# Kernel tuning notes

Hardware: AMD Instinct MI355X
Metric: run time of the kernel (lower is better)

Reference implementation:

```python
import jax, jax.numpy as jnp
import numpy as np

N = 10000      # nodes
E = 320000     # edges (before self-loops)
D = 256        # d_model
DC = 128       # d_content = d_model // 2
L = 3          # num_layers
K = 4096       # nodes_of_interest
LN_EPS = 1e-5


def setup_inputs() -> dict:
    key = jax.random.key(0)
    ks = jax.random.split(key, 7)
    x = jax.random.normal(ks[0], (N, D), dtype=jnp.float32)
    edge_index = jax.random.randint(ks[1], (2, E), 0, N)
    nodes_of_interest = jax.random.randint(ks[2], (K,), 0, N)
    # per-layer linear weights (stacked over layers)
    Wc = jax.random.normal(ks[3], (L, DC, DC), dtype=jnp.float32) * (1.0 / np.sqrt(DC))
    bc = jnp.zeros((L, DC), dtype=jnp.float32)
    Wp = jax.random.normal(ks[4], (L, DC, DC), dtype=jnp.float32) * (1.0 / np.sqrt(DC))
    bp = jnp.zeros((L, DC), dtype=jnp.float32)
    gamma = jnp.ones((L, D), dtype=jnp.float32)
    beta = jnp.zeros((L, D), dtype=jnp.float32)
    return {"x": x, "edge_index": edge_index, "nodes_of_interest": nodes_of_interest,
            "Wc": Wc, "bc": bc, "Wp": Wp, "bp": bp, "gamma": gamma, "beta": beta}


def _layernorm(h, g, b):
    mu = jnp.mean(h, axis=-1, keepdims=True)
    var = jnp.mean((h - mu) ** 2, axis=-1, keepdims=True)
    return (h - mu) * jax.lax.rsqrt(var + LN_EPS) * g + b


def reference(x, edge_index, nodes_of_interest, Wc, bc, Wp, bp, gamma, beta):
    n = x.shape[0]
    loops = jnp.arange(n)
    # add self-loops (PyG add_self_loops): done per conv in torch but identical each layer
    row = jnp.concatenate([edge_index[0], loops])  # source j
    col = jnp.concatenate([edge_index[1], loops])  # target i
    # symmetric-ish normalization: degree counted over row only (as in source)
    deg = jax.ops.segment_sum(jnp.ones_like(row, dtype=x.dtype), row, num_segments=n)
    dis = deg ** -0.5
    norm = dis[row] * dis[col]  # [E+N]

    def conv(h, l):
        hc = h[:, :DC] @ Wc[l].T + bc[l]
        hp = h[:, DC:] @ Wp[l].T + bp[l]
        ht = jnp.concatenate([hc, hp], axis=-1)
        msg = norm[:, None] * ht[row]                      # gather + normalize
        return jax.ops.segment_sum(msg, col, num_segments=n)  # scatter-add

    for l in range(L - 1):
        x = x + jax.nn.relu(_layernorm(conv(x, l), gamma[l], beta[l]))
    x = x + _layernorm(conv(x, L - 1), gamma[L - 1], beta[L - 1])
    return x[nodes_of_interest]
```

## Files before the change

### kernel.cpp

```cpp
#include <hip/hip_runtime.h>

#define DMODEL 256
#define DCH 128
#define NLAYER 3
#define LN_EPS 1e-5f

typedef float f32x4 __attribute__((ext_vector_type(4)));
typedef short s16x8 __attribute__((ext_vector_type(8)));

__device__ __forceinline__ unsigned short f2bf(float f) {
  unsigned int u = __float_as_uint(f);
  unsigned int r = (u + 0x7FFF + ((u >> 16) & 1)) >> 16;
  return (unsigned short)r;
}
__device__ __forceinline__ unsigned int pk2bf(float x, float y) {
  return ((unsigned int)f2bf(y) << 16) | f2bf(x);
}
__device__ __forceinline__ float bflo(unsigned int u) { return __uint_as_float(u << 16); }
__device__ __forceinline__ float bfhi(unsigned int u) { return __uint_as_float(u & 0xFFFF0000u); }

__global__ __launch_bounds__(256) void hist_cvt_kernel(
    const int* __restrict__ row, const int* __restrict__ col,
    int* cnt_row, int* cnt_col, int E,
    const float* __restrict__ x, unsigned short* __restrict__ xbf, int nx8,
    const float* __restrict__ Wc, unsigned short* __restrict__ Wcb,
    const float* __restrict__ Wp, unsigned short* __restrict__ Wpb, int nw8) {
  int tid = blockIdx.x * 256 + threadIdx.x;
  if (tid < E) {
    atomicAdd(&cnt_row[row[tid]], 1);
    atomicAdd(&cnt_col[col[tid]], 1);
  }
  if (tid < nx8) {
    float4 a = *(const float4*)&x[tid * 8];
    float4 b = *(const float4*)&x[tid * 8 + 4];
    uint4 o = {pk2bf(a.x, a.y), pk2bf(a.z, a.w), pk2bf(b.x, b.y), pk2bf(b.z, b.w)};
    *(uint4*)&xbf[tid * 8] = o;
  }
  if (tid < nw8) {
    float4 a = *(const float4*)&Wc[tid * 8];
    float4 b = *(const float4*)&Wc[tid * 8 + 4];
    uint4 o = {pk2bf(a.x, a.y), pk2bf(a.z, a.w), pk2bf(b.x, b.y), pk2bf(b.z, b.w)};
    *(uint4*)&Wcb[tid * 8] = o;
    a = *(const float4*)&Wp[tid * 8];
    b = *(const float4*)&Wp[tid * 8 + 4];
    uint4 o2 = {pk2bf(a.x, a.y), pk2bf(a.z, a.w), pk2bf(b.x, b.y), pk2bf(b.z, b.w)};
    *(uint4*)&Wpb[tid * 8] = o2;
  }
}

__global__ __launch_bounds__(256) void scan_dis_kernel(
    const int* __restrict__ cnt_col, const int* __restrict__ cnt_row,
    int* __restrict__ indptr, int* __restrict__ cursor,
    float* __restrict__ dis, int N, int E) {
  int t = threadIdx.x;
  for (int i = t; i < N; i += 256) dis[i] = rsqrtf((float)(cnt_row[i] + 1));
  const int PER = (N + 255) / 256;
  int start = t * PER;
  int sum = 0;
  for (int k = 0; k < PER; ++k) {
    int i = start + k;
    if (i < N) sum += cnt_col[i];
  }
  int lane = t & 63, wid = t >> 6;
  int inc = sum;
#pragma unroll
  for (int off = 1; off < 64; off <<= 1) {
    int v = __shfl_up(inc, off);
    if (lane >= off) inc += v;
  }
  __shared__ int wsum[4];
  if (lane == 63) wsum[wid] = inc;
  __syncthreads();
  int woff = 0;
  for (int w = 0; w < wid; ++w) woff += wsum[w];
  int run = woff + inc - sum;
  for (int k = 0; k < PER; ++k) {
    int i = start + k;
    if (i < N) {
      indptr[i] = run;
      cursor[i] = run;
      run += cnt_col[i];
    }
  }
  if (t == 255) indptr[N] = E;
}

__global__ __launch_bounds__(256) void fill_kernel(const int* __restrict__ row,
    const int* __restrict__ col, int* cursor, int* __restrict__ idx, int E) {
  int e = blockIdx.x * 256 + threadIdx.x;
  if (e < E) {
    int pos = atomicAdd(&cursor[col[e]], 1);
    idx[pos] = row[e];
  }
}

__global__ __launch_bounds__(256) void agg_kernel(
    const unsigned short* __restrict__ xbf, unsigned short* __restrict__ S,
    float* __restrict__ swt, const float* __restrict__ dis,
    const int* __restrict__ indptr, const int* __restrict__ idx,
    const int* __restrict__ noi, int use_noi, int R) {
  int wave = threadIdx.x >> 6, lane = threadIdx.x & 63;
  int r = blockIdx.x * 4 + wave;
  int rc = min(r, R - 1);
  int i = use_noi ? noi[rc] : rc;
  float di = dis[i];
  float di2 = di * di;

  uint2 u = *(const uint2*)(xbf + (size_t)i * DMODEL + lane * 4);
  float a0 = di2 * bflo(u.x), a1 = di2 * bfhi(u.x);
  float a2 = di2 * bflo(u.y), a3 = di2 * bfhi(u.y);

  int s = indptr[i], e = indptr[i + 1];
  float sw = 0.f;
  for (int base = s; base < e; base += 64) {
    int n = min(64, e - base);
    int sr = 0;
    float w = 0.f;
    if (lane < n) {
      sr = idx[base + lane];
      w = dis[sr] * di;
    }
    int j = 0;
    for (; j + 4 <= n; j += 4) {
      int s0 = __shfl(sr, j), s1 = __shfl(sr, j + 1), s2 = __shfl(sr, j + 2), s3 = __shfl(sr, j + 3);
      float w0 = __shfl(w, j), w1 = __shfl(w, j + 1), w2 = __shfl(w, j + 2), w3 = __shfl(w, j + 3);
      uint2 u0 = *(const uint2*)(xbf + (size_t)s0 * DMODEL + lane * 4);
      uint2 u1 = *(const uint2*)(xbf + (size_t)s1 * DMODEL + lane * 4);
      uint2 u2 = *(const uint2*)(xbf + (size_t)s2 * DMODEL + lane * 4);
      uint2 u3 = *(const uint2*)(xbf + (size_t)s3 * DMODEL + lane * 4);
      a0 += w0 * bflo(u0.x); a1 += w0 * bfhi(u0.x); a2 += w0 * bflo(u0.y); a3 += w0 * bfhi(u0.y);
      a0 += w1 * bflo(u1.x); a1 += w1 * bfhi(u1.x); a2 += w1 * bflo(u1.y); a3 += w1 * bfhi(u1.y);
      a0 += w2 * bflo(u2.x); a1 += w2 * bfhi(u2.x); a2 += w2 * bflo(u2.y); a3 += w2 * bfhi(u2.y);
      a0 += w3 * bflo(u3.x); a1 += w3 * bfhi(u3.x); a2 += w3 * bflo(u3.y); a3 += w3 * bfhi(u3.y);
      sw += w0 + w1 + w2 + w3;
    }
    for (; j < n; ++j) {
      int sj = __shfl(sr, j);
      float wj = __shfl(w, j);
      uint2 uu = *(const uint2*)(xbf + (size_t)sj * DMODEL + lane * 4);
      a0 += wj * bflo(uu.x); a1 += wj * bfhi(uu.x); a2 += wj * bflo(uu.y); a3 += wj * bfhi(uu.y);
      sw += wj;
    }
  }
  if (r < R) {
    uint2 o = {pk2bf(a0, a1), pk2bf(a2, a3)};
    *(uint2*)(S + (size_t)r * DMODEL + lane * 4) = o;
    if (lane == 0) swt[r] = di2 + sw;
  }
}

__global__ __launch_bounds__(512) void xform_kernel(
    const unsigned short* __restrict__ S, const float* __restrict__ swt,
    const unsigned short* __restrict__ Wcb, const unsigned short* __restrict__ Wpb,
    const float* __restrict__ bc, const float* __restrict__ bp,
    const float* __restrict__ gamma, const float* __restrict__ beta,
    const float* __restrict__ xin, const int* __restrict__ noi,
    float* __restrict__ xout, unsigned short* __restrict__ xbf_out,
    int use_noi, int relu, int R) {
  int t = threadIdx.x;
  int w = t >> 6, lane = t & 63;
  int mt = w & 1, cq = w >> 1;
  int h = cq >> 1, cgg = cq & 1;
  int lrow = lane & 15, kgrp = lane >> 4;
  int r0 = blockIdx.x * 32;

  int arow = r0 + mt * 16 + lrow;
  int arow_c = min(arow, R - 1);
  const unsigned short* ap = S + (size_t)arow_c * DMODEL + h * DCH + kgrp * 8;
  const unsigned short* Wh = h ? Wpb : Wcb;
  const float* bh = h ? bp : bc;

  int orow0 = mt * 16 + kgrp * 4;
  float sj[4];
#pragma unroll
  for (int j = 0; j < 4; ++j) sj[j] = swt[min(r0 + orow0 + j, R - 1)];

  int colw[4];
  const unsigned short* bpw[4];
  f32x4 acc[4];
#pragma unroll
  for (int nt = 0; nt < 4; ++nt) {
    colw[nt] = cgg * 64 + nt * 16 + lrow;
    bpw[nt] = Wh + (size_t)colw[nt] * DCH + kgrp * 8;
    float bias = bh[colw[nt]];
    acc[nt] = (f32x4){bias * sj[0], bias * sj[1], bias * sj[2], bias * sj[3]};
  }

  union U8 { s16x8 v; uint4 q; };
#pragma unroll
  for (int kt = 0; kt < 4; ++kt) {
    U8 af;
    af.q = *(const uint4*)(ap + kt * 32);
#pragma unroll
    for (int nt = 0; nt < 4; ++nt) {
      U8 bf;
      bf.q = *(const uint4*)(bpw[nt] + kt * 32);
      acc[nt] = __builtin_amdgcn_mfma_f32_16x16x32_bf16(af.v, bf.v, acc[nt], 0, 0, 0);
    }
  }

  float p1[4], p2[4];
#pragma unroll
  for (int j = 0; j < 4; ++j) {
    p1[j] = acc[0][j] + acc[1][j] + acc[2][j] + acc[3][j];
    p2[j] = acc[0][j] * acc[0][j] + acc[1][j] * acc[1][j] +
            acc[2][j] * acc[2][j] + acc[3][j] * acc[3][j];
  }
#pragma unroll
  for (int off = 8; off > 0; off >>= 1) {
#pragma unroll
    for (int j = 0; j < 4; ++j) {
      p1[j] += __shfl_down(p1[j], off, 16);
      p2[j] += __shfl_down(p2[j], off, 16);
    }
  }
  __shared__ float red1[32][4], red2[32][4];
  __shared__ float muS[32], rsS[32];
  if (lrow == 0) {
#pragma unroll
    for (int j = 0; j < 4; ++j) {
      red1[orow0 + j][cq] = p1[j];
      red2[orow0 + j][cq] = p2[j];
    }
  }
  __syncthreads();
  if (t < 32) {
    float s1 = red1[t][0] + red1[t][1] + red1[t][2] + red1[t][3];
    float s2 = red2[t][0] + red2[t][1] + red2[t][2] + red2[t][3];
    float mu = s1 * (1.0f / DMODEL);
    float var = s2 * (1.0f / DMODEL) - mu * mu;
    muS[t] = mu;
    rsS[t] = rsqrtf(var + LN_EPS);
  }
  __syncthreads();

#pragma unroll
  for (int nt = 0; nt < 4; ++nt) {
    int col = h * DCH + colw[nt];
    float g = gamma[col], bt = beta[col];
#pragma unroll
    for (int j = 0; j < 4; ++j) {
      int rr = orow0 + j;
      int grow = r0 + rr;
      if (grow < R) {
        float y = (acc[nt][j] - muS[rr]) * rsS[rr] * g + bt;
        if (relu) y = fmaxf(y, 0.f);
        int node = use_noi ? noi[grow] : grow;
        float o = xin[(size_t)node * DMODEL + col] + y;
        xout[(size_t)grow * DMODEL + col] = o;
        if (xbf_out) xbf_out[(size_t)grow * DMODEL + col] = f2bf(o);
      }
    }
  }
}

extern "C" void kernel_launch(void* const* d_in, const int* in_sizes, int n_in,
                              void* d_out, int out_size, void* d_ws, size_t ws_size,
                              hipStream_t stream) {
  const float* x     = (const float*)d_in[0];
  const int*   edges = (const int*)d_in[1];
  const int*   noi   = (const int*)d_in[2];
  const float* Wc    = (const float*)d_in[3];
  const float* bc    = (const float*)d_in[4];
  const float* Wp    = (const float*)d_in[5];
  const float* bp    = (const float*)d_in[6];
  const float* gamma = (const float*)d_in[7];
  const float* beta  = (const float*)d_in[8];

  int N = in_sizes[0] / DMODEL;
  int E = in_sizes[1] / 2;
  int K = in_sizes[2];
  int nwElem = in_sizes[3];
  const int* row = edges;
  const int* col = edges + E;

  char* base = (char*)d_ws;
  size_t off = 0;
  auto alloc = [&](size_t bytes) -> void* {
    void* p = base + off;
    off += (bytes + 255) & ~(size_t)255;
    return p;
  };

  unsigned short* xbf0   = (unsigned short*)alloc((size_t)N * DMODEL * 2);
  unsigned short* xbfA   = (unsigned short*)alloc((size_t)N * DMODEL * 2);
  unsigned short* xbfB   = (unsigned short*)alloc((size_t)N * DMODEL * 2);
  unsigned short* Sb     = (unsigned short*)alloc((size_t)N * DMODEL * 2);
  float*          xA     = (float*)alloc((size_t)N * DMODEL * 4);
  float*          xB     = (float*)alloc((size_t)N * DMODEL * 4);
  unsigned short* Wcb    = (unsigned short*)alloc((size_t)nwElem * 2);
  unsigned short* Wpb    = (unsigned short*)alloc((size_t)nwElem * 2);
  float*          swt    = (float*)alloc((size_t)N * 4);
  float*          dis    = (float*)alloc((size_t)N * 4);
  int*            cnt    = (int*)alloc((size_t)2 * N * 4);
  int*            indptr = (int*)alloc((size_t)(N + 1) * 4);
  int*            cursor = (int*)alloc((size_t)N * 4);
  int*            idx    = (int*)alloc((size_t)E * 4);

  hipMemsetAsync(cnt, 0, (size_t)2 * N * 4, stream);

  int nx8 = (N * DMODEL) / 8;
  int nw8 = nwElem / 8;
  int mx = E > nx8 ? E : nx8;
  if (nw8 > mx) mx = nw8;
  hist_cvt_kernel<<<(mx + 255) / 256, 256, 0, stream>>>(
      row, col, cnt, cnt + N, E, x, xbf0, nx8, Wc, Wcb, Wp, Wpb, nw8);
  scan_dis_kernel<<<1, 256, 0, stream>>>(cnt + N, cnt, indptr, cursor, dis, N, E);
  fill_kernel<<<(E + 255) / 256, 256, 0, stream>>>(row, col, cursor, idx, E);

  agg_kernel<<<(N + 3) / 4, 256, 0, stream>>>(xbf0, Sb, swt, dis, indptr, idx, nullptr, 0, N);
  xform_kernel<<<(N + 31) / 32, 512, 0, stream>>>(
      Sb, swt, Wcb, Wpb, bc, bp, gamma, beta, x, nullptr, xA, xbfA, 0, 1, N);
  agg_kernel<<<(N + 3) / 4, 256, 0, stream>>>(xbfA, Sb, swt, dis, indptr, idx, nullptr, 0, N);
  xform_kernel<<<(N + 31) / 32, 512, 0, stream>>>(
      Sb, swt, Wcb + (size_t)DCH * DCH, Wpb + (size_t)DCH * DCH, bc + DCH, bp + DCH,
      gamma + DMODEL, beta + DMODEL, xA, nullptr, xB, xbfB, 0, 1, N);
  agg_kernel<<<(K + 3) / 4, 256, 0, stream>>>(xbfB, Sb, swt, dis, indptr, idx, noi, 1, K);
  xform_kernel<<<(K + 31) / 32, 512, 0, stream>>>(
      Sb, swt, Wcb + (size_t)2 * DCH * DCH, Wpb + (size_t)2 * DCH * DCH, bc + 2 * DCH, bp + 2 * DCH,
      gamma + 2 * DMODEL, beta + 2 * DMODEL, xB, noi, (float*)d_out, nullptr, 1, 0, K);
}
```

Measured before the change: 265.5 us.

## Fuse neighbor aggregation and linear/LayerNorm transform into one per-layer kernel

Merges the gather-aggregate kernel and the MFMA transform+LayerNorm kernel into a single layer kernel. Each 512-thread block aggregates its 32 rows into LDS, where each wave handles 4 rows, and then runs the bf16 MFMA transform directly from that padded LDS tile. This removes the global round-trip of the aggregated S buffer and the swt buffer, plus three kernel launches. In exchange, each block has fewer independent gather waves in flight per row and higher LDS use, which could lower occupancy or latency hiding for the gather phase.

```diff
diff --git a/kernel.cpp b/kernel.cpp
--- a/kernel.cpp
+++ b/kernel.cpp
@@ -2,8 +2,8 @@
 
 #define DMODEL 256
 #define DCH 128
-#define NLAYER 3
 #define LN_EPS 1e-5f
+#define SROW (DMODEL + 8)
 
 typedef float f32x4 __attribute__((ext_vector_type(4)));
 typedef short s16x8 __attribute__((ext_vector_type(8)));
@@ -94,86 +94,85 @@
   }
 }
 
-__global__ __launch_bounds__(256) void agg_kernel(
-    const unsigned short* __restrict__ xbf, unsigned short* __restrict__ S,
-    float* __restrict__ swt, const float* __restrict__ dis,
-    const int* __restrict__ indptr, const int* __restrict__ idx,
-    const int* __restrict__ noi, int use_noi, int R) {
-  int wave = threadIdx.x >> 6, lane = threadIdx.x & 63;
-  int r = blockIdx.x * 4 + wave;
-  int rc = min(r, R - 1);
-  int i = use_noi ? noi[rc] : rc;
-  float di = dis[i];
-  float di2 = di * di;
-
-  uint2 u = *(const uint2*)(xbf + (size_t)i * DMODEL + lane * 4);
-  float a0 = di2 * bflo(u.x), a1 = di2 * bfhi(u.x);
-  float a2 = di2 * bflo(u.y), a3 = di2 * bfhi(u.y);
-
-  int s = indptr[i], e = indptr[i + 1];
-  float sw = 0.f;
-  for (int base = s; base < e; base += 64) {
-    int n = min(64, e - base);
-    int sr = 0;
-    float w = 0.f;
-    if (lane < n) {
-      sr = idx[base + lane];
-      w = dis[sr] * di;
-    }
-    int j = 0;
-    for (; j + 4 <= n; j += 4) {
-      int s0 = __shfl(sr, j), s1 = __shfl(sr, j + 1), s2 = __shfl(sr, j + 2), s3 = __shfl(sr, j + 3);
-      float w0 = __shfl(w, j), w1 = __shfl(w, j + 1), w2 = __shfl(w, j + 2), w3 = __shfl(w, j + 3);
-      uint2 u0 = *(const uint2*)(xbf + (size_t)s0 * DMODEL + lane * 4);
-      uint2 u1 = *(const uint2*)(xbf + (size_t)s1 * DMODEL + lane * 4);
-      uint2 u2 = *(const uint2*)(xbf + (size_t)s2 * DMODEL + lane * 4);
-      uint2 u3 = *(const uint2*)(xbf + (size_t)s3 * DMODEL + lane * 4);
-      a0 += w0 * bflo(u0.x); a1 += w0 * bfhi(u0.x); a2 += w0 * bflo(u0.y); a3 += w0 * bfhi(u0.y);
-      a0 += w1 * bflo(u1.x); a1 += w1 * bfhi(u1.x); a2 += w1 * bflo(u1.y); a3 += w1 * bfhi(u1.y);
-      a0 += w2 * bflo(u2.x); a1 += w2 * bfhi(u2.x); a2 += w2 * bflo(u2.y); a3 += w2 * bfhi(u2.y);
-      a0 += w3 * bflo(u3.x); a1 += w3 * bfhi(u3.x); a2 += w3 * bflo(u3.y); a3 += w3 * bfhi(u3.y);
-      sw += w0 + w1 + w2 + w3;
-    }
-    for (; j < n; ++j) {
-      int sj = __shfl(sr, j);
-      float wj = __shfl(w, j);
-      uint2 uu = *(const uint2*)(xbf + (size_t)sj * DMODEL + lane * 4);
-      a0 += wj * bflo(uu.x); a1 += wj * bfhi(uu.x); a2 += wj * bflo(uu.y); a3 += wj * bfhi(uu.y);
-      sw += wj;
-    }
-  }
-  if (r < R) {
-    uint2 o = {pk2bf(a0, a1), pk2bf(a2, a3)};
-    *(uint2*)(S + (size_t)r * DMODEL + lane * 4) = o;
-    if (lane == 0) swt[r] = di2 + sw;
-  }
-}
-
-__global__ __launch_bounds__(512) void xform_kernel(
-    const unsigned short* __restrict__ S, const float* __restrict__ swt,
+__global__ __launch_bounds__(512) void layer_kernel(
+    const unsigned short* __restrict__ xbf, const float* __restrict__ xres,
     const unsigned short* __restrict__ Wcb, const unsigned short* __restrict__ Wpb,
     const float* __restrict__ bc, const float* __restrict__ bp,
     const float* __restrict__ gamma, const float* __restrict__ beta,
-    const float* __restrict__ xin, const int* __restrict__ noi,
+    const float* __restrict__ dis, const int* __restrict__ indptr,
+    const int* __restrict__ idx, const int* __restrict__ noi,
     float* __restrict__ xout, unsigned short* __restrict__ xbf_out,
     int use_noi, int relu, int R) {
+  __shared__ unsigned short S_lds[32][SROW];
+  __shared__ float swt_lds[32];
+  __shared__ float red1[32][4], red2[32][4], muS[32], rsS[32];
+
   int t = threadIdx.x;
   int w = t >> 6, lane = t & 63;
+  int r0 = blockIdx.x * 32;
+
+  for (int q = 0; q < 4; ++q) {
+    int lr = w * 4 + q;
+    int r = r0 + lr;
+    if (r < R) {
+      int i = use_noi ? noi[r] : r;
+      float di = dis[i];
+      float di2 = di * di;
+      uint2 u = *(const uint2*)(xbf + (size_t)i * DMODEL + lane * 4);
+      float a0 = di2 * bflo(u.x), a1 = di2 * bfhi(u.x);
+      float a2 = di2 * bflo(u.y), a3 = di2 * bfhi(u.y);
+      int s = indptr[i], e = indptr[i + 1];
+      float sw = 0.f;
+      for (int base = s; base < e; base += 64) {
+        int n = min(64, e - base);
+        int sr = 0;
+        float wt = 0.f;
+        if (lane < n) {
+          sr = idx[base + lane];
+          wt = dis[sr] * di;
+        }
+        int j = 0;
+        for (; j + 4 <= n; j += 4) {
+          int s0 = __shfl(sr, j), s1 = __shfl(sr, j + 1), s2 = __shfl(sr, j + 2), s3 = __shfl(sr, j + 3);
+          float w0 = __shfl(wt, j), w1 = __shfl(wt, j + 1), w2 = __shfl(wt, j + 2), w3 = __shfl(wt, j + 3);
+          uint2 u0 = *(const uint2*)(xbf + (size_t)s0 * DMODEL + lane * 4);
+          uint2 u1 = *(const uint2*)(xbf + (size_t)s1 * DMODEL + lane * 4);
+          uint2 u2 = *(const uint2*)(xbf + (size_t)s2 * DMODEL + lane * 4);
+          uint2 u3 = *(const uint2*)(xbf + (size_t)s3 * DMODEL + lane * 4);
+          a0 += w0 * bflo(u0.x); a1 += w0 * bfhi(u0.x); a2 += w0 * bflo(u0.y); a3 += w0 * bfhi(u0.y);
+          a0 += w1 * bflo(u1.x); a1 += w1 * bfhi(u1.x); a2 += w1 * bflo(u1.y); a3 += w1 * bfhi(u1.y);
+          a0 += w2 * bflo(u2.x); a1 += w2 * bfhi(u2.x); a2 += w2 * bflo(u2.y); a3 += w2 * bfhi(u2.y);
+          a0 += w3 * bflo(u3.x); a1 += w3 * bfhi(u3.x); a2 += w3 * bflo(u3.y); a3 += w3 * bfhi(u3.y);
+          sw += w0 + w1 + w2 + w3;
+        }
+        for (; j < n; ++j) {
+          int sj_ = __shfl(sr, j);
+          float wj = __shfl(wt, j);
+          uint2 uu = *(const uint2*)(xbf + (size_t)sj_ * DMODEL + lane * 4);
+          a0 += wj * bflo(uu.x); a1 += wj * bfhi(uu.x); a2 += wj * bflo(uu.y); a3 += wj * bfhi(uu.y);
+          sw += wj;
+        }
+      }
+      *(uint2*)&S_lds[lr][lane * 4] = (uint2){pk2bf(a0, a1), pk2bf(a2, a3)};
+      if (lane == 0) swt_lds[lr] = di2 + sw;
+    } else {
+      *(uint2*)&S_lds[lr][lane * 4] = (uint2){0u, 0u};
+      if (lane == 0) swt_lds[lr] = 0.f;
+    }
+  }
+  __syncthreads();
+
   int mt = w & 1, cq = w >> 1;
   int h = cq >> 1, cgg = cq & 1;
   int lrow = lane & 15, kgrp = lane >> 4;
-  int r0 = blockIdx.x * 32;
-
-  int arow = r0 + mt * 16 + lrow;
-  int arow_c = min(arow, R - 1);
-  const unsigned short* ap = S + (size_t)arow_c * DMODEL + h * DCH + kgrp * 8;
+
+  int orow0 = mt * 16 + kgrp * 4;
+  float sj[4];
+#pragma unroll
+  for (int j = 0; j < 4; ++j) sj[j] = swt_lds[orow0 + j];
+
   const unsigned short* Wh = h ? Wpb : Wcb;
   const float* bh = h ? bp : bc;
-
-  int orow0 = mt * 16 + kgrp * 4;
-  float sj[4];
-#pragma unroll
-  for (int j = 0; j < 4; ++j) sj[j] = swt[min(r0 + orow0 + j, R - 1)];
 
   int colw[4];
   const unsigned short* bpw[4];
@@ -186,6 +185,8 @@
     acc[nt] = (f32x4){bias * sj[0], bias * sj[1], bias * sj[2], bias * sj[3]};
   }
 
+  const unsigned short* ap = &S_lds[mt * 16 + lrow][h * DCH + kgrp * 8];
+
   union U8 { s16x8 v; uint4 q; };
 #pragma unroll
   for (int kt = 0; kt < 4; ++kt) {
@@ -214,8 +215,6 @@
       p2[j] += __shfl_down(p2[j], off, 16);
     }
   }
-  __shared__ float red1[32][4], red2[32][4];
-  __shared__ float muS[32], rsS[32];
   if (lrow == 0) {
 #pragma unroll
     for (int j = 0; j < 4; ++j) {
@@ -246,7 +245,7 @@
         float y = (acc[nt][j] - muS[rr]) * rsS[rr] * g + bt;
         if (relu) y = fmaxf(y, 0.f);
         int node = use_noi ? noi[grow] : grow;
-        float o = xin[(size_t)node * DMODEL + col] + y;
+        float o = xres[(size_t)node * DMODEL + col] + y;
         xout[(size_t)grow * DMODEL + col] = o;
         if (xbf_out) xbf_out[(size_t)grow * DMODEL + col] = f2bf(o);
       }
@@ -285,12 +284,10 @@
   unsigned short* xbf0   = (unsigned short*)alloc((size_t)N * DMODEL * 2);
   unsigned short* xbfA   = (unsigned short*)alloc((size_t)N * DMODEL * 2);
   unsigned short* xbfB   = (unsigned short*)alloc((size_t)N * DMODEL * 2);
-  unsigned short* Sb     = (unsigned short*)alloc((size_t)N * DMODEL * 2);
   float*          xA     = (float*)alloc((size_t)N * DMODEL * 4);
   float*          xB     = (float*)alloc((size_t)N * DMODEL * 4);
   unsigned short* Wcb    = (unsigned short*)alloc((size_t)nwElem * 2);
   unsigned short* Wpb    = (unsigned short*)alloc((size_t)nwElem * 2);
-  float*          swt    = (float*)alloc((size_t)N * 4);
   float*          dis    = (float*)alloc((size_t)N * 4);
   int*            cnt    = (int*)alloc((size_t)2 * N * 4);
   int*            indptr = (int*)alloc((size_t)(N + 1) * 4);
@@ -308,15 +305,16 @@
   scan_dis_kernel<<<1, 256, 0, stream>>>(cnt + N, cnt, indptr, cursor, dis, N, E);
   fill_kernel<<<(E + 255) / 256, 256, 0, stream>>>(row, col, cursor, idx, E);
 
-  agg_kernel<<<(N + 3) / 4, 256, 0, stream>>>(xbf0, Sb, swt, dis, indptr, idx, nullptr, 0, N);
-  xform_kernel<<<(N + 31) / 32, 512, 0, stream>>>(
-      Sb, swt, Wcb, Wpb, bc, bp, gamma, beta, x, nullptr, xA, xbfA, 0, 1, N);
-  agg_kernel<<<(N + 3) / 4, 256, 0, stream>>>(xbfA, Sb, swt, dis, indptr, idx, nullptr, 0, N);
-  xform_kernel<<<(N + 31) / 32, 512, 0, stream>>>(
-      Sb, swt, Wcb + (size_t)DCH * DCH, Wpb + (size_t)DCH * DCH, bc + DCH, bp + DCH,
-      gamma + DMODEL, beta + DMODEL, xA, nullptr, xB, xbfB, 0, 1, N);
-  agg_kernel<<<(K + 3) / 4, 256, 0, stream>>>(xbfB, Sb, swt, dis, indptr, idx, noi, 1, K);
-  xform_kernel<<<(K + 31) / 32, 512, 0, stream>>>(
-      Sb, swt, Wcb + (size_t)2 * DCH * DCH, Wpb + (size_t)2 * DCH * DCH, bc + 2 * DCH, bp + 2 * DCH,
-      gamma + 2 * DMODEL, beta + 2 * DMODEL, xB, noi, (float*)d_out, nullptr, 1, 0, K);
-}
+  size_t wl = (size_t)DCH * DCH;
+  layer_kernel<<<(N + 31) / 32, 512, 0, stream>>>(
+      xbf0, x, Wcb, Wpb, bc, bp, gamma, beta, dis, indptr, idx, nullptr,
+      xA, xbfA, 0, 1, N);
+  layer_kernel<<<(N + 31) / 32, 512, 0, stream>>>(
+      xbfA, xA, Wcb + wl, Wpb + wl, bc + DCH, bp + DCH,
+      gamma + DMODEL, beta + DMODEL, dis, indptr, idx, nullptr,
+      xB, xbfB, 0, 1, N);
+  layer_kernel<<<(K + 31) / 32, 512, 0, stream>>>(
+      xbfB, xB, Wcb + 2 * wl, Wpb + 2 * wl, bc + 2 * DCH, bp + 2 * DCH,
+      gamma + 2 * DMODEL, beta + 2 * DMODEL, dis, indptr, idx, noi,
+      (float*)d_out, nullptr, 1, 0, K);
+}
```

Result: slower. 284.2 us (+7.0%).
